# Kernel tuning notes

Measured on AMD Instinct MI355X. Metric: run time of the kernel, lower is better.

The kernel has to match this reference:

```python
import jax, jax.numpy as jnp
import numpy as np

B, D, M = 512, 1024, 32768
K, MULTI_K, AUX_K = 32, 128, 64
DEAD_THRESH = 256
MATRYOSHKA_SIZES = [4096, 16384, 32768]


def setup_inputs() -> dict:
    key = jax.random.key(0)
    k0, k1, k2, k3, k4, k5 = jax.random.split(key, 6)
    return {
        "x": jax.random.normal(k0, (B, D), dtype=jnp.float32),
        "W_enc": jax.random.normal(k1, (M, D), dtype=jnp.float32) * 0.02,
        "W_dec": jax.random.normal(k2, (D, M), dtype=jnp.float32) * 0.02,
        "input_bias": jax.random.normal(k3, (D,), dtype=jnp.float32) * 0.01,
        "neuron_bias": jax.random.normal(k4, (M,), dtype=jnp.float32) * 0.01,
        "steps_since_activation": jax.random.randint(k5, (M,), 0, 512, dtype=jnp.int64),
    }


def reference(x, W_enc, W_dec, input_bias, neuron_bias, steps_since_activation):
    xc = x - input_bias                                   # [B, D]
    pre_act = xc @ W_enc.T + neuron_bias                  # [B, M]

    topk_values, topk_indices = jax.lax.top_k(pre_act, K)
    topk_values = jax.nn.relu(topk_values)
    multik_values, multik_indices = jax.lax.top_k(pre_act, MULTI_K)
    multik_values = jax.nn.relu(multik_values)

    rows = jnp.arange(pre_act.shape[0])[:, None]
    activations = jnp.zeros_like(pre_act).at[rows, topk_indices].set(topk_values)
    multik_activations = jnp.zeros_like(pre_act).at[rows, multik_indices].set(multik_values)

    reconstruction = activations @ W_dec.T + input_bias
    multik_reconstruction = multik_activations @ W_dec.T + input_bias

    # matryoshka partial reconstructions (all sizes except the last/full one)
    neuron_ids = jnp.arange(M)
    matryoshka_recons = []
    for m_i in MATRYOSHKA_SIZES[:-1]:
        partial_acts = activations * (neuron_ids < m_i).astype(activations.dtype)
        matryoshka_recons.append(partial_acts @ W_dec.T + input_bias)

    # aux-k over dead neurons (steps incremented by 1 before the mask in torch)
    dead_mask = ((steps_since_activation + 1) > DEAD_THRESH).astype(pre_act.dtype)
    aux_values, aux_indices = jax.lax.top_k(pre_act * dead_mask, AUX_K)
    aux_values = jax.nn.relu(aux_values)

    return (reconstruction, multik_reconstruction,
            matryoshka_recons[0], matryoshka_recons[1],
            topk_indices, topk_values, aux_indices, aux_values)
```

## Files before the change

### kernel.cpp

```cpp
#include <hip/hip_runtime.h>
#include <stdint.h>

#define B_ 512
#define D_ 1024
#define M_ 32768

typedef _Float16 half8 __attribute__((ext_vector_type(8)));
typedef _Float16 half4 __attribute__((ext_vector_type(4)));
typedef float f32x4 __attribute__((ext_vector_type(4)));

__device__ __forceinline__ unsigned f2k(float f) {
    unsigned b = __float_as_uint(f);
    return (b & 0x80000000u) ? ~b : (b | 0x80000000u);
}
__device__ __forceinline__ float k2f(unsigned k) {
    unsigned b = (k & 0x80000000u) ? (k & 0x7FFFFFFFu) : ~k;
    return __uint_as_float(b);
}
__device__ __forceinline__ unsigned long long d2k(double d) {
    unsigned long long b = (unsigned long long)__double_as_longlong(d);
    return (b & 0x8000000000000000ull) ? ~b : (b | 0x8000000000000000ull);
}

__device__ __forceinline__ void gld16(const void* g, void* l) {
    __builtin_amdgcn_global_load_lds(
        (__attribute__((address_space(1))) void*)(uintptr_t)g,
        (__attribute__((address_space(3))) void*)(unsigned)(uintptr_t)l,
        16, 0, 0);
}

__global__ __launch_bounds__(256) void split_x_k(
    const float* __restrict__ x, const float* __restrict__ ib,
    _Float16* __restrict__ xh)
{
    int i = blockIdx.x * 256 + threadIdx.x;
    float4 v = ((const float4*)x)[i];
    float4 bb = ((const float4*)ib)[i & 255];
    float a0 = (v.x - bb.x) * 2048.0f;
    float a1 = (v.y - bb.y) * 2048.0f;
    float a2 = (v.z - bb.z) * 2048.0f;
    float a3 = (v.w - bb.w) * 2048.0f;
    half4 hv = {(_Float16)a0, (_Float16)a1, (_Float16)a2, (_Float16)a3};
    ((half4*)xh)[i] = hv;
}

__global__ __launch_bounds__(256, 6) void enc_tr(
    const _Float16* __restrict__ xhf,
    const float* __restrict__ wenc, const float* __restrict__ nb,
    _Float16* __restrict__ preact,
    const float* __restrict__ wdec, _Float16* __restrict__ wdt)
{
    __shared__ alignas(16) char smem[24576];

    const int tid = threadIdx.x;
    const int chunk = blockIdx.x >> 8;
    const int sub = (chunk >> 1) * 256 + (blockIdx.x & 255);

    if (chunk & 1) {
        float* tile = (float*)smem;
        const int r = tid >> 2;
        const int q4 = (tid & 3) * 16;
        for (int s = 0; s < 4; ++s) {
            int tix = sub * 4 + s;
            int x0 = (tix & 511) * 64;
            int y0 = (tix >> 9) * 64;
            const float* src = wdec + (size_t)(y0 + r) * M_ + x0 + q4;
            float4 v0 = *(const float4*)(src + 0);
            float4 v1 = *(const float4*)(src + 4);
            float4 v2 = *(const float4*)(src + 8);
            float4 v3 = *(const float4*)(src + 12);
            float* dst = &tile[r * 65 + q4];
            dst[0] = v0.x;  dst[1] = v0.y;  dst[2] = v0.z;  dst[3] = v0.w;
            dst[4] = v1.x;  dst[5] = v1.y;  dst[6] = v1.z;  dst[7] = v1.w;
            dst[8] = v2.x;  dst[9] = v2.y;  dst[10] = v2.z; dst[11] = v2.w;
            dst[12] = v3.x; dst[13] = v3.y; dst[14] = v3.z; dst[15] = v3.w;
            __syncthreads();
            half8 h0, h1;
#pragma unroll
            for (int i = 0; i < 8; ++i) h0[i] = (_Float16)tile[(q4 + i) * 65 + r];
#pragma unroll
            for (int i = 0; i < 8; ++i) h1[i] = (_Float16)tile[(q4 + 8 + i) * 65 + r];
            _Float16* od = wdt + (size_t)(x0 + r) * D_ + y0 + q4;
            *(half8*)(od + 0) = h0;
            *(half8*)(od + 8) = h1;
            __syncthreads();
        }
        return;
    }

    _Float16* lA0 = (_Float16*)smem;
    _Float16* lB0 = (_Float16*)(smem + 16384);

    const int lane = tid & 63;
    const int wv = tid >> 6;
    const int wvr = wv >> 1;
    const int wvc = wv & 1;

    const int bid = sub;
    const int lb = bid >> 3;
    const int j0 = ((bid & 7) * 64 + (lb >> 2)) * 64;
    const int i0 = (lb & 3) * 128;

    const int ln15 = lane & 15;
    const int kq = (lane >> 4) * 8;

    f32x4 acc1[4][2];
#pragma unroll
    for (int r = 0; r < 4; ++r)
#pragma unroll
        for (int c = 0; c < 2; ++c)
            acc1[r][c] = (f32x4){0.f, 0.f, 0.f, 0.f};

    const int o0 = tid * 16;
    const int o1 = o0 + 4096;
    const int rA0 = o0 >> 6, rA1 = o1 >> 6;
    const int cA0s = (o0 & 63) ^ (((rA0 >> 1) & 3) << 4);
    const int cA1s = (o1 & 63) ^ (((rA1 >> 1) & 3) << 4);

    const int rW = tid >> 2;
    const int c8 = (tid & 3) * 8;
    const int c8s = c8 ^ (((rW >> 1) & 3) << 3);

    const int rowA = wvr * 64 + ln15;
    const int rowB = wvc * 32 + ln15;

#define STAGEA(k0, s)                                                                      \
    do {                                                                                   \
        gld16((const char*)(xhf + (size_t)(i0 + rA0) * 1024 + (k0)) + cA0s, (char*)lA0 + (s) * 8192 + o0); \
        gld16((const char*)(xhf + (size_t)(i0 + rA1) * 1024 + (k0)) + cA1s, (char*)lA0 + (s) * 8192 + o1); \
    } while (0)

#define LOADB(k0)                                                                          \
    do {                                                                                   \
        const float* wp = wenc + (size_t)(j0 + rW) * 1024 + (k0) + c8;                     \
        wv0 = *(const float4*)wp;                                                          \
        wv1 = *(const float4*)(wp + 4);                                                    \
    } while (0)

#define CVT1(idx, f) do { bh[idx] = (_Float16)((f) * 2048.0f); } while (0)

#define WRITEB(s)                                                                          \
    do {                                                                                   \
        half8 bh;                                                                          \
        CVT1(0, wv0.x); CVT1(1, wv0.y); CVT1(2, wv0.z); CVT1(3, wv0.w);                    \
        CVT1(4, wv1.x); CVT1(5, wv1.y); CVT1(6, wv1.z); CVT1(7, wv1.w);                    \
        *(half8*)&lB0[(s) * 2048 + rW * 32 + c8s] = bh;                                    \
    } while (0)

    float4 wv0, wv1;
    LOADB(0);
    asm volatile("s_waitcnt vmcnt(0)" ::: "memory");
    WRITEB(0);
    STAGEA(0, 0);
    LOADB(32);
    STAGEA(32, 1);
    asm volatile("s_waitcnt vmcnt(2)" ::: "memory");
    WRITEB(1);
    asm volatile("s_waitcnt lgkmcnt(0)" ::: "memory");
    __builtin_amdgcn_s_barrier();

    int cur = 0;
    for (int k0 = 0; k0 < 1024; k0 += 32) {
        if (k0 + 64 < 1024) LOADB(k0 + 64);

        half8 aH[4], bH[2];
#pragma unroll
        for (int r = 0; r < 4; ++r) {
            const int ra = rowA + r * 16;
            const int ka = kq ^ (((ra >> 1) & 3) << 3);
            aH[r] = *(const half8*)&lA0[cur * 4096 + ra * 32 + ka];
        }
#pragma unroll
        for (int c = 0; c < 2; ++c) {
            const int rb = rowB + c * 16;
            const int kb = kq ^ (((rb >> 1) & 3) << 3);
            bH[c] = *(const half8*)&lB0[cur * 2048 + rb * 32 + kb];
        }
#pragma unroll
        for (int r = 0; r < 4; ++r)
#pragma unroll
            for (int c = 0; c < 2; ++c)
                acc1[r][c] = __builtin_amdgcn_mfma_f32_16x16x32_f16(aH[r], bH[c], acc1[r][c], 0, 0, 0);

        if (k0 + 32 < 1024) {
            asm volatile("s_waitcnt lgkmcnt(0)" ::: "memory");
            __builtin_amdgcn_s_barrier();

            if (k0 + 64 < 1024) {
                STAGEA(k0 + 64, cur);
                asm volatile("s_waitcnt vmcnt(2)" ::: "memory");
                WRITEB(cur);
            } else {
                asm volatile("s_waitcnt vmcnt(0)" ::: "memory");
            }
            asm volatile("s_waitcnt lgkmcnt(0)" ::: "memory");
            __builtin_amdgcn_s_barrier();
        }
        cur ^= 1;
    }
#undef STAGEA
#undef LOADB
#undef CVT1
#undef WRITEB

    asm volatile("s_waitcnt lgkmcnt(0)" ::: "memory");
    __builtin_amdgcn_s_barrier();
    _Float16* ct = (_Float16*)smem;
    const float s1 = 0x1p-22f;
#pragma unroll
    for (int c = 0; c < 2; ++c) {
        int n = wvc * 32 + c * 16 + ln15;
        float nbv = nb[j0 + n];
#pragma unroll
        for (int r = 0; r < 4; ++r) {
            int mb = wvr * 64 + r * 16 + (lane >> 4) * 4;
#pragma unroll
            for (int e = 0; e < 4; ++e)
                ct[(mb + e) * 64 + n] = (_Float16)(acc1[r][c][e] * s1 + nbv);
        }
    }
    __syncthreads();
#pragma unroll
    for (int s = 0; s < 4; ++s) {
        int idx = s * 256 + tid;
        int row = idx >> 3;
        int off8 = (idx & 7) * 8;
        *(half8*)(preact + (size_t)(i0 + row) * M_ + j0 + off8) = *(half8*)&ct[row * 64 + off8];
    }
}

__global__ __launch_bounds__(1024, 2) void selresdec(
    const _Float16* __restrict__ preact, const int* __restrict__ steps,
    const float* __restrict__ x, const float* __restrict__ ib,
    const float* __restrict__ wenc, const float* __restrict__ nb,
    const _Float16* __restrict__ wdt,
    float* __restrict__ out_tidx, float* __restrict__ out_tval,
    float* __restrict__ out_aidx, float* __restrict__ out_aval,
    float* __restrict__ o_recon, float* __restrict__ o_multik,
    float* __restrict__ o_mat0, float* __restrict__ o_mat1)
{
    __shared__ unsigned histU[4096];
    __shared__ unsigned histM[4096];
    __shared__ unsigned coarseU[256];
    __shared__ unsigned coarseM[256];
    __shared__ unsigned long long candU[512];
    __shared__ unsigned long long candM[512];
    __shared__ double xcs[1024];
    __shared__ double part[160][4];
    __shared__ unsigned long long kU[64];
    __shared__ unsigned long long kM[128];
    __shared__ float vU[64];
    __shared__ float vM[128];
    __shared__ int sidx[128];
    __shared__ float sval[128];
    __shared__ int auxm[96];
    __shared__ int ridx[32];
    __shared__ float rval[32];
    __shared__ unsigned cntU, cntM, thrU, thrM, cbU, cbM, cumU, cumM;

    const int t = threadIdx.x;
    const int b = blockIdx.x;
    const half8* rowh = (const half8*)(preact + (size_t)b * M_);

    for (int i = t; i < 4096; i += 1024) { histU[i] = 0; histM[i] = 0; }
    if (t < 512) { candU[t] = 0ULL; candM[t] = 0ULL; }
    if (t == 0) { cntU = 0; cntM = 0; }
    xcs[t] = (double)x[(size_t)b * 1024 + t] - (double)ib[t];
    if (t < 64)  { kU[t] = 0ULL; vU[t] = 0.f; }
    if (t < 128) { kM[t] = 0ULL; vM[t] = 0.f; }
    __syncthreads();

    unsigned deadmask = 0;
#pragma unroll
    for (int p = 0; p < 4; ++p) {
        int base = 2 * t + 2048 * p;
        int4 s0 = ((const int4*)steps)[base];
        int4 s1 = ((const int4*)steps)[base + 1];
        unsigned mb = 0;
        if (s0.x + 1 > 256) mb |= 1u;
        if (s0.y + 1 > 256) mb |= 2u;
        if (s0.z + 1 > 256) mb |= 4u;
        if (s0.w + 1 > 256) mb |= 8u;
        if (s1.x + 1 > 256) mb |= 16u;
        if (s1.y + 1 > 256) mb |= 32u;
        if (s1.z + 1 > 256) mb |= 64u;
        if (s1.w + 1 > 256) mb |= 128u;
        deadmask |= mb << (p * 8);
    }

    half8 v[4];
#pragma unroll
    for (int p = 0; p < 4; ++p) {
        v[p] = rowh[t + p * 1024];
#pragma unroll
        for (int e = 0; e < 8; ++e) {
            unsigned key = f2k((float)v[p][e]) >> 20;
            atomicAdd(&histU[key], 1u);
            if ((deadmask >> (p * 8 + e)) & 1u) atomicAdd(&histM[key], 1u);
        }
    }
    __syncthreads();

    if (t < 256) {
        unsigned s = 0;
#pragma unroll
        for (int j = 0; j < 16; ++j) s += histU[t * 16 + j];
        coarseU[t] = s;
    } else if (t < 512) {
        int c = t - 256;
        unsigned s = 0;
#pragma unroll
        for (int j = 0; j < 16; ++j) s += histM[c * 16 + j];
        coarseM[c] = s;
    }
    __syncthreads();

    for (int off = 1; off < 256; off <<= 1) {
        unsigned xv = 0;
        if (t < 256)      xv = coarseU[t] + (t + off < 256 ? coarseU[t + off] : 0u);
        else if (t < 512) { int c = t - 256; xv = coarseM[c] + (c + off < 256 ? coarseM[c + off] : 0u); }
        __syncthreads();
        if (t < 256)      coarseU[t] = xv;
        else if (t < 512) coarseM[t - 256] = xv;
        __syncthreads();
    }

    if (t < 256) {
        unsigned S = coarseU[t];
        unsigned Sn = (t < 255) ? coarseU[t + 1] : 0u;
        if (S >= 128u && (t == 255 || Sn < 128u)) { cbU = (unsigned)t; cumU = Sn; }
    } else if (t < 512) {
        int c = t - 256;
        unsigned S = coarseM[c];
        unsigned Sn = (c < 255) ? coarseM[c + 1] : 0u;
        if (S >= 64u && (c == 255 || Sn < 64u)) { cbM = (unsigned)c; cumM = Sn; }
        if (c == 0 && S < 64u) { cbM = 0u; cumM = Sn; }
    }
    __syncthreads();

    if (t == 0) {
        unsigned cum = cumU;
        int base = (int)cbU * 16, tb = base;
        for (int f = base + 15; f >= base; --f) {
            unsigned h = histU[f];
            if (cum + h >= 128u) { tb = f; break; }
            cum += h;
        }
        thrU = (unsigned)tb;
    }
    if (t == 64) {
        unsigned cum = cumM;
        int base = (int)cbM * 16, tb = base;
        for (int f = base + 15; f >= base; --f) {
            unsigned h = histM[f];
            if (cum + h >= 64u) { tb = f; break; }
            cum += h;
        }
        thrM = (unsigned)(tb > 0 ? tb - 1 : 0);
    }
    __syncthreads();

    const unsigned TU = thrU, TM = thrM;

#pragma unroll
    for (int p = 0; p < 4; ++p) {
#pragma unroll
        for (int e = 0; e < 8; ++e) {
            float val = (float)v[p][e];
            unsigned key = f2k(val);
            int m = (t + p * 1024) * 8 + e;
            if ((key >> 20) >= TU) {
                unsigned pz = atomicAdd(&cntU, 1u);
                if (pz < 512u) candU[pz] = ((unsigned long long)key << 32) | (unsigned)(~m);
            }
            if (((deadmask >> (p * 8 + e)) & 1u) && (key >> 20) >= TM) {
                unsigned pz = atomicAdd(&cntM, 1u);
                if (pz < 512u) candM[pz] = ((unsigned long long)key << 32) | (unsigned)(~m);
            }
        }
    }
    __syncthreads();

    {
        unsigned long long* arr = (t < 512) ? candU : candM;
        const unsigned i = (unsigned)t & 511u;
        for (unsigned kk = 2; kk <= 512; kk <<= 1) {
            for (unsigned j = kk >> 1; j > 0; j >>= 1) {
                unsigned ixj = i ^ j;
                if (ixj > i) {
                    bool desc = ((i & kk) == 0);
                    unsigned long long a = arr[i], c = arr[ixj];
                    if (desc ? (a < c) : (a > c)) { arr[i] = c; arr[ixj] = a; }
                }
                unsigned nj = (j > 1) ? (j >> 1) : ((kk << 1) <= 512u ? kk : 0u);
                if (j >= 64 || nj >= 64) __syncthreads();
                else asm volatile("s_waitcnt lgkmcnt(0)" ::: "memory");
            }
        }
    }
    __syncthreads();

    if (t < 128) {
        unsigned long long c = candU[t];
        unsigned m = ~(unsigned)c;
        float vv = k2f((unsigned)(c >> 32));
        sidx[t] = (int)m;
        sval[t] = vv > 0.f ? vv : 0.f;
    }
    if (t < 96) {
        unsigned long long c = candM[t];
        auxm[t] = c ? (int)(~(unsigned)c) : -1;
    }
    __syncthreads();

    if (t < 640) {
        const int ci = t >> 2, q = t & 3;
        int m = (ci < 64) ? sidx[ci] : auxm[ci - 64];
        if (m >= 0) {
            const float* w = wenc + (size_t)m * 1024 + q * 256;
            const double* xq = xcs + q * 256;
            double a0 = 0.0, a1 = 0.0, a2 = 0.0, a3 = 0.0;
            for (int d = 0; d < 256; d += 4) {
                float4 wv = *(const float4*)(w + d);
                a0 = fma((double)wv.x, xq[d + 0], a0);
                a1 = fma((double)wv.y, xq[d + 1], a1);
                a2 = fma((double)wv.z, xq[d + 2], a2);
                a3 = fma((double)wv.w, xq[d + 3], a3);
            }
            part[ci][q] = ((a0 + a1) + (a2 + a3));
        }
    }
    __syncthreads();

    if (t < 160) {
        int m = (t < 64) ? sidx[t] : auxm[t - 64];
        if (m >= 0) {
            double vd = ((part[t][0] + part[t][1]) + (part[t][2] + part[t][3])) + (double)nb[m];
            unsigned long long key = (d2k(vd) & 0xFFFFFFFFFFFF0000ull)
                                   | (unsigned long long)((~(unsigned)m) & 0xFFFFu);
            float vf = (float)vd;
            if (t < 64) { kU[t] = key; vU[t] = vf; }
            else        { kM[t - 64] = key; vM[t - 64] = vf; }
        }
    }
    __syncthreads();

    for (unsigned kk = 2; kk <= 128; kk <<= 1) {
        for (unsigned j = kk >> 1; j > 0; j >>= 1) {
            unsigned i = (unsigned)t, ixj = i ^ j;
            if (kk <= 64 && i < 64 && ixj > i) {
                bool desc = ((i & kk) == 0);
                unsigned long long a = kU[i], c = kU[ixj];
                if (desc ? (a < c) : (a > c)) {
                    kU[i] = c; kU[ixj] = a;
                    float fa = vU[i]; vU[i] = vU[ixj]; vU[ixj] = fa;
                }
            }
            if (i < 128 && ixj > i) {
                bool desc = ((i & kk) == 0);
                unsigned long long a = kM[i], c = kM[ixj];
                if (desc ? (a < c) : (a > c)) {
                    kM[i] = c; kM[ixj] = a;
                    float fa = vM[i]; vM[i] = vM[ixj]; vM[ixj] = fa;
                }
            }
            __syncthreads();
        }
    }

    if (t < 32) {
        unsigned mm = (~(unsigned)kU[t]) & 0xFFFFu;
        float vv = vU[t];
        float rv = vv > 0.f ? vv : 0.f;
        ridx[t] = (int)mm;
        rval[t] = rv;
        out_tidx[b * 32 + t] = (float)mm;
        out_tval[b * 32 + t] = rv;
    }
    if (t < 64) {
        unsigned mm = (~(unsigned)kM[t]) & 0xFFFFu;
        float vv = vM[t];
        out_aidx[b * 64 + t] = (float)mm;
        out_aval[b * 64 + t] = vv > 0.f ? vv : 0.f;
    }
    __syncthreads();

    {
        const int d = t;
        float bias = ib[d];
        float mul = bias, rec = bias, m0 = bias, m1 = bias;
        for (int k = 0; k < 128; ++k) {
            float vv = sval[k];
            float w = (float)wdt[(size_t)sidx[k] * D_ + d];
            mul += vv * w;
        }
        for (int k = 0; k < 32; ++k) {
            int idx = ridx[k];
            float vv = rval[k];
            float w = (float)wdt[(size_t)idx * D_ + d];
            rec += vv * w;
            if (idx < 16384) {
                m1 += vv * w;
                if (idx < 4096) m0 += vv * w;
            }
        }
        size_t o = (size_t)b * D_ + d;
        o_recon[o]  = rec;
        o_multik[o] = mul;
        o_mat0[o]   = m0;
        o_mat1[o]   = m1;
    }
}

extern "C" void kernel_launch(void* const* d_in, const int* in_sizes, int n_in,
                              void* d_out, int out_size, void* d_ws, size_t ws_size,
                              hipStream_t stream)
{
    const float* x     = (const float*)d_in[0];
    const float* wenc  = (const float*)d_in[1];
    const float* wdec  = (const float*)d_in[2];
    const float* ib    = (const float*)d_in[3];
    const float* nb    = (const float*)d_in[4];
    const int*   steps = (const int*)d_in[5];
    float* out = (float*)d_out;

    char* ws = (char*)d_ws;
    _Float16*  preact  = (_Float16*)ws;
    _Float16*  wdt     = (_Float16*)(ws + 67108864);
    _Float16*  xhf     = (_Float16*)(ws + 201326592);

    float* out_recon  = out;
    float* out_multik = out + 524288;
    float* out_mat0   = out + 1048576;
    float* out_mat1   = out + 1572864;
    float* out_tidx   = out + 2097152;
    float* out_tval   = out + 2097152 + 16384;
    float* out_aidx   = out + 2097152 + 32768;
    float* out_aval   = out + 2097152 + 32768 + 32768;

    split_x_k<<<dim3(512), dim3(256), 0, stream>>>(x, ib, xhf);
    enc_tr<<<dim3(4096), dim3(256), 0, stream>>>(xhf, wenc, nb, preact, wdec, wdt);
    selresdec<<<dim3(512), dim3(1024), 0, stream>>>(
        preact, steps, x, ib, wenc, nb, wdt,
        out_tidx, out_tval, out_aidx, out_aval,
        out_recon, out_multik, out_mat0, out_mat1);
}
```

Before: 487.8 us.

## Widen encoder GEMM tile to 128x128 and shrink fp64 refine candidate counts

The encoder GEMM blocks now compute 128x128 output tiles instead of 128x64, so each block loads twice as many W_enc rows. This halves the number of GEMM blocks and raises data reuse per block. The block interleaving with the W_dec transpose work changes to a 1:2 pattern and the grid shrinks accordingly. Launch bounds drop to 3 waves/SIMD to fit the larger accumulators. Separately, the fp64 rescoring stage now refines 48 top-k and 80 aux candidates, splitting each dot product across 8 threads instead of 4. Fewer candidates may risk correctness when fp16 ranking errors push true top-k members past the reduced margin.

```diff
diff --git a/kernel.cpp b/kernel.cpp
--- a/kernel.cpp
+++ b/kernel.cpp
@@ -44,19 +44,19 @@
     ((half4*)xh)[i] = hv;
 }
 
-__global__ __launch_bounds__(256, 6) void enc_tr(
+__global__ __launch_bounds__(256, 3) void enc_tr(
     const _Float16* __restrict__ xhf,
     const float* __restrict__ wenc, const float* __restrict__ nb,
     _Float16* __restrict__ preact,
     const float* __restrict__ wdec, _Float16* __restrict__ wdt)
 {
-    __shared__ alignas(16) char smem[24576];
+    __shared__ alignas(16) char smem[32768];
 
     const int tid = threadIdx.x;
     const int chunk = blockIdx.x >> 8;
-    const int sub = (chunk >> 1) * 256 + (blockIdx.x & 255);
-
-    if (chunk & 1) {
+
+    if (chunk % 3 != 0) {
+        const int sub = (chunk - 1 - chunk / 3) * 256 + (blockIdx.x & 255);
         float* tile = (float*)smem;
         const int r = tid >> 2;
         const int q4 = (tid & 3) * 16;
@@ -91,24 +91,24 @@
     _Float16* lA0 = (_Float16*)smem;
     _Float16* lB0 = (_Float16*)(smem + 16384);
 
+    const int sub = (chunk / 3) * 256 + (blockIdx.x & 255);
     const int lane = tid & 63;
     const int wv = tid >> 6;
     const int wvr = wv >> 1;
     const int wvc = wv & 1;
 
-    const int bid = sub;
-    const int lb = bid >> 3;
-    const int j0 = ((bid & 7) * 64 + (lb >> 2)) * 64;
+    const int lb = sub >> 3;
+    const int j0 = ((sub & 7) * 32 + (lb >> 2)) * 128;
     const int i0 = (lb & 3) * 128;
 
     const int ln15 = lane & 15;
     const int kq = (lane >> 4) * 8;
 
-    f32x4 acc1[4][2];
+    f32x4 acc1[4][4];
 #pragma unroll
     for (int r = 0; r < 4; ++r)
 #pragma unroll
-        for (int c = 0; c < 2; ++c)
+        for (int c = 0; c < 4; ++c)
             acc1[r][c] = (f32x4){0.f, 0.f, 0.f, 0.f};
 
     const int o0 = tid * 16;
@@ -117,12 +117,14 @@
     const int cA0s = (o0 & 63) ^ (((rA0 >> 1) & 3) << 4);
     const int cA1s = (o1 & 63) ^ (((rA1 >> 1) & 3) << 4);
 
-    const int rW = tid >> 2;
-    const int c8 = (tid & 3) * 8;
-    const int c8s = c8 ^ (((rW >> 1) & 3) << 3);
+    const int rW = tid >> 1;
+    const int c16 = (tid & 1) * 16;
+    const int sw = ((rW >> 1) & 3) << 3;
+    const int g0 = c16 ^ sw;
+    const int g1 = (c16 + 8) ^ sw;
 
     const int rowA = wvr * 64 + ln15;
-    const int rowB = wvc * 32 + ln15;
+    const int rowB = wvc * 64 + ln15;
 
 #define STAGEA(k0, s)                                                                      \
     do {                                                                                   \
@@ -132,22 +134,29 @@
 
 #define LOADB(k0)                                                                          \
     do {                                                                                   \
-        const float* wp = wenc + (size_t)(j0 + rW) * 1024 + (k0) + c8;                     \
+        const float* wp = wenc + (size_t)(j0 + rW) * 1024 + (k0) + c16;                    \
         wv0 = *(const float4*)wp;                                                          \
         wv1 = *(const float4*)(wp + 4);                                                    \
+        wv2 = *(const float4*)(wp + 8);                                                    \
+        wv3 = *(const float4*)(wp + 12);                                                   \
     } while (0)
-
-#define CVT1(idx, f) do { bh[idx] = (_Float16)((f) * 2048.0f); } while (0)
 
 #define WRITEB(s)                                                                          \
     do {                                                                                   \
-        half8 bh;                                                                          \
-        CVT1(0, wv0.x); CVT1(1, wv0.y); CVT1(2, wv0.z); CVT1(3, wv0.w);                    \
-        CVT1(4, wv1.x); CVT1(5, wv1.y); CVT1(6, wv1.z); CVT1(7, wv1.w);                    \
-        *(half8*)&lB0[(s) * 2048 + rW * 32 + c8s] = bh;                                    \
+        half8 b0, b1;                                                                      \
+        b0[0] = (_Float16)(wv0.x * 2048.0f); b0[1] = (_Float16)(wv0.y * 2048.0f);          \
+        b0[2] = (_Float16)(wv0.z * 2048.0f); b0[3] = (_Float16)(wv0.w * 2048.0f);          \
+        b0[4] = (_Float16)(wv1.x * 2048.0f); b0[5] = (_Float16)(wv1.y * 2048.0f);          \
+        b0[6] = (_Float16)(wv1.z * 2048.0f); b0[7] = (_Float16)(wv1.w * 2048.0f);          \
+        b1[0] = (_Float16)(wv2.x * 2048.0f); b1[1] = (_Float16)(wv2.y * 2048.0f);          \
+        b1[2] = (_Float16)(wv2.z * 2048.0f); b1[3] = (_Float16)(wv2.w * 2048.0f);          \
+        b1[4] = (_Float16)(wv3.x * 2048.0f); b1[5] = (_Float16)(wv3.y * 2048.0f);          \
+        b1[6] = (_Float16)(wv3.z * 2048.0f); b1[7] = (_Float16)(wv3.w * 2048.0f);          \
+        *(half8*)&lB0[(s) * 4096 + rW * 32 + g0] = b0;                                     \
+        *(half8*)&lB0[(s) * 4096 + rW * 32 + g1] = b1;                                     \
     } while (0)
 
-    float4 wv0, wv1;
+    float4 wv0, wv1, wv2, wv3;
     LOADB(0);
     asm volatile("s_waitcnt vmcnt(0)" ::: "memory");
     WRITEB(0);
@@ -163,7 +172,7 @@
     for (int k0 = 0; k0 < 1024; k0 += 32) {
         if (k0 + 64 < 1024) LOADB(k0 + 64);
 
-        half8 aH[4], bH[2];
+        half8 aH[4], bH[4];
 #pragma unroll
         for (int r = 0; r < 4; ++r) {
             const int ra = rowA + r * 16;
@@ -171,15 +180,15 @@
             aH[r] = *(const half8*)&lA0[cur * 4096 + ra * 32 + ka];
         }
 #pragma unroll
-        for (int c = 0; c < 2; ++c) {
+        for (int c = 0; c < 4; ++c) {
             const int rb = rowB + c * 16;
             const int kb = kq ^ (((rb >> 1) & 3) << 3);
-            bH[c] = *(const half8*)&lB0[cur * 2048 + rb * 32 + kb];
+            bH[c] = *(const half8*)&lB0[cur * 4096 + rb * 32 + kb];
         }
 #pragma unroll
         for (int r = 0; r < 4; ++r)
 #pragma unroll
-            for (int c = 0; c < 2; ++c)
+            for (int c = 0; c < 4; ++c)
                 acc1[r][c] = __builtin_amdgcn_mfma_f32_16x16x32_f16(aH[r], bH[c], acc1[r][c], 0, 0, 0);
 
         if (k0 + 32 < 1024) {
@@ -200,7 +209,6 @@
     }
 #undef STAGEA
 #undef LOADB
-#undef CVT1
 #undef WRITEB
 
     asm volatile("s_waitcnt lgkmcnt(0)" ::: "memory");
@@ -208,24 +216,24 @@
     _Float16* ct = (_Float16*)smem;
     const float s1 = 0x1p-22f;
 #pragma unroll
-    for (int c = 0; c < 2; ++c) {
-        int n = wvc * 32 + c * 16 + ln15;
+    for (int c = 0; c < 4; ++c) {
+        int n = wvc * 64 + c * 16 + ln15;
         float nbv = nb[j0 + n];
 #pragma unroll
         for (int r = 0; r < 4; ++r) {
             int mb = wvr * 64 + r * 16 + (lane >> 4) * 4;
 #pragma unroll
             for (int e = 0; e < 4; ++e)
-                ct[(mb + e) * 64 + n] = (_Float16)(acc1[r][c][e] * s1 + nbv);
-        }
-    }
-    __syncthreads();
-#pragma unroll
-    for (int s = 0; s < 4; ++s) {
+                ct[(mb + e) * 128 + n] = (_Float16)(acc1[r][c][e] * s1 + nbv);
+        }
+    }
+    __syncthreads();
+#pragma unroll
+    for (int s = 0; s < 8; ++s) {
         int idx = s * 256 + tid;
-        int row = idx >> 3;
-        int off8 = (idx & 7) * 8;
-        *(half8*)(preact + (size_t)(i0 + row) * M_ + j0 + off8) = *(half8*)&ct[row * 64 + off8];
+        int row = idx >> 4;
+        int off8 = (idx & 15) * 8;
+        *(half8*)(preact + (size_t)(i0 + row) * M_ + j0 + off8) = *(half8*)&ct[row * 128 + off8];
     }
 }
 
@@ -246,14 +254,14 @@
     __shared__ unsigned long long candU[512];
     __shared__ unsigned long long candM[512];
     __shared__ double xcs[1024];
-    __shared__ double part[160][4];
+    __shared__ double part[128][8];
     __shared__ unsigned long long kU[64];
     __shared__ unsigned long long kM[128];
     __shared__ float vU[64];
     __shared__ float vM[128];
     __shared__ int sidx[128];
     __shared__ float sval[128];
-    __shared__ int auxm[96];
+    __shared__ int auxm[80];
     __shared__ int ridx[32];
     __shared__ float rval[32];
     __shared__ unsigned cntU, cntM, thrU, thrM, cbU, cbM, cumU, cumM;
@@ -407,20 +415,20 @@
         sidx[t] = (int)m;
         sval[t] = vv > 0.f ? vv : 0.f;
     }
-    if (t < 96) {
+    if (t < 80) {
         unsigned long long c = candM[t];
         auxm[t] = c ? (int)(~(unsigned)c) : -1;
     }
     __syncthreads();
 
-    if (t < 640) {
-        const int ci = t >> 2, q = t & 3;
-        int m = (ci < 64) ? sidx[ci] : auxm[ci - 64];
+    {
+        const int ci = t >> 3, q = t & 7;
+        int m = (ci < 48) ? sidx[ci] : auxm[ci - 48];
         if (m >= 0) {
-            const float* w = wenc + (size_t)m * 1024 + q * 256;
-            const double* xq = xcs + q * 256;
+            const float* w = wenc + (size_t)m * 1024 + q * 128;
+            const double* xq = xcs + q * 128;
             double a0 = 0.0, a1 = 0.0, a2 = 0.0, a3 = 0.0;
-            for (int d = 0; d < 256; d += 4) {
+            for (int d = 0; d < 128; d += 4) {
                 float4 wv = *(const float4*)(w + d);
                 a0 = fma((double)wv.x, xq[d + 0], a0);
                 a1 = fma((double)wv.y, xq[d + 1], a1);
@@ -432,15 +440,17 @@
     }
     __syncthreads();
 
-    if (t < 160) {
-        int m = (t < 64) ? sidx[t] : auxm[t - 64];
+    if (t < 128) {
+        int m = (t < 48) ? sidx[t] : auxm[t - 48];
         if (m >= 0) {
-            double vd = ((part[t][0] + part[t][1]) + (part[t][2] + part[t][3])) + (double)nb[m];
+            double vd = (((part[t][0] + part[t][1]) + (part[t][2] + part[t][3]))
+                       + ((part[t][4] + part[t][5]) + (part[t][6] + part[t][7])))
+                      + (double)nb[m];
             unsigned long long key = (d2k(vd) & 0xFFFFFFFFFFFF0000ull)
                                    | (unsigned long long)((~(unsigned)m) & 0xFFFFu);
             float vf = (float)vd;
-            if (t < 64) { kU[t] = key; vU[t] = vf; }
-            else        { kM[t - 64] = key; vM[t - 64] = vf; }
+            if (t < 48) { kU[t] = key; vU[t] = vf; }
+            else        { kM[t - 48] = key; vM[t - 48] = vf; }
         }
     }
     __syncthreads();
@@ -539,7 +549,7 @@
     float* out_aval   = out + 2097152 + 32768 + 32768;
 
     split_x_k<<<dim3(512), dim3(256), 0, stream>>>(x, ib, xhf);
-    enc_tr<<<dim3(4096), dim3(256), 0, stream>>>(xhf, wenc, nb, preact, wdec, wdt);
+    enc_tr<<<dim3(3072), dim3(256), 0, stream>>>(xhf, wenc, nb, preact, wdec, wdt);
     selresdec<<<dim3(512), dim3(1024), 0, stream>>>(
         preact, steps, x, ib, wenc, nb, wdt,
         out_tidx, out_tval, out_aidx, out_aval,
```

New measurement: 480.0 us. No clear change (-1.6%).
